# Kernel tuning notes

Hardware: AMD Instinct MI355X
Metric: run time of the kernel (lower is better)

The kernel has to match this reference:

```python
import jax, jax.numpy as jnp
import numpy as np

B, S, H, P = 4, 4096, 1024, 10

def setup_inputs() -> dict:
    key = jax.random.key(0)
    k1, k2, k3, k4, k5 = jax.random.split(key, 5)
    return {
        "query": jax.random.normal(k1, (B, S, H), dtype=jnp.float32),
        "key": jax.random.normal(k2, (B, S, H), dtype=jnp.float32),
        "value": jax.random.normal(k3, (B, S, H), dtype=jnp.float32),
        "prefix_k": jax.random.normal(k4, (P, H), dtype=jnp.float32),
        "prefix_v": jax.random.normal(k5, (P, H), dtype=jnp.float32),
    }

def reference(query, key, value, prefix_k, prefix_v):
    # Broadcast learned prefix over batch and concat ahead of real K/V.
    b = query.shape[0]
    pk = jnp.broadcast_to(prefix_k[None], (b,) + prefix_k.shape)  # [B, P, H]
    pv = jnp.broadcast_to(prefix_v[None], (b,) + prefix_v.shape)
    k_all = jnp.concatenate([pk, key], axis=1)    # [B, P+S, H]
    v_all = jnp.concatenate([pv, value], axis=1)  # [B, P+S, H]
    # Raw (unscaled, unmasked) attention, exactly as the torch module does.
    scores = jnp.einsum("bqh,bkh->bqk", query, k_all)  # [B, S, P+S]
    attn = jax.nn.softmax(scores, axis=-1)
    return jnp.einsum("bqk,bkh->bqh", attn, v_all)     # [B, S, H]
```

## Files before the change

### kernel.cpp

```cpp
#include <hip/hip_runtime.h>
#include <cstdint>
#include <cstddef>

#define BB 4
#define SS 4096
#define HH 1024
#define PP 10
#define LL 4106
#define NTILES 129
#define CHUNKS_PB (NTILES * 4096)
#define TILE_ELEMS (4096 * 8)
#define LOG2E 1.44269504088896f

typedef __attribute__((ext_vector_type(8))) _Float16 half8v;
typedef __attribute__((ext_vector_type(4))) float float4v;

union hu16 { _Float16 h; unsigned short u; };

__device__ __forceinline__ half8v cvt8h(float4v f0, float4v f1) {
  half8v h;
  h[0] = (_Float16)f0[0]; h[1] = (_Float16)f0[1];
  h[2] = (_Float16)f0[2]; h[3] = (_Float16)f0[3];
  h[4] = (_Float16)f1[0]; h[5] = (_Float16)f1[1];
  h[6] = (_Float16)f1[2]; h[7] = (_Float16)f1[3];
  return h;
}
__device__ __forceinline__ unsigned pack2h(float a, float b) {
  hu16 x, y; x.h = (_Float16)a; y.h = (_Float16)b;
  return (unsigned)x.u | ((unsigned)y.u << 16);
}

#define LGKM_BAR() do { \
  asm volatile("s_waitcnt lgkmcnt(0)" ::: "memory"); \
  __builtin_amdgcn_s_barrier(); \
  asm volatile("" ::: "memory"); } while (0)

__global__ __launch_bounds__(256) void conv_k(const float* __restrict__ prefix_k,
                                              const float* __restrict__ key,
                                              _Float16* __restrict__ kp) {
  const int b = blockIdx.y;
  const int id = blockIdx.x * 256 + threadIdx.x;
  const int li = id & 15, g = (id >> 4) & 3, ktp = (id >> 6) & 31,
            nt = (id >> 11) & 1, it = id >> 12;
  const int n = it * 32 + nt * 16 + li;
  const int d = ktp * 32 + g * 8;
  float4v f0 = {0.f, 0.f, 0.f, 0.f}, f1 = {0.f, 0.f, 0.f, 0.f};
  if (n < LL) {
    const float* src = (n < PP) ? prefix_k + (size_t)n * HH + d
                                : key + ((size_t)b * SS + (n - PP)) * HH + d;
    f0 = *(const float4v*)src; f1 = *(const float4v*)(src + 4);
  }
  *(half8v*)(kp + ((size_t)b * CHUNKS_PB + id) * 8) = cvt8h(f0, f1);
}

__global__ __launch_bounds__(256) void conv_v(const float* __restrict__ prefix_v,
                                              const float* __restrict__ value,
                                              _Float16* __restrict__ vp) {
  const int b = blockIdx.y;
  const int id = blockIdx.x * 256 + threadIdx.x;
  const int d = id & 1023, g = (id >> 10) & 3, it = id >> 12;
  const int nb = it * 32 + g * 8;
  half8v h;
  #pragma unroll
  for (int j = 0; j < 8; ++j) {
    int n = nb + j;
    float f = 0.f;
    if (n < LL)
      f = (n < PP) ? prefix_v[(size_t)n * HH + d]
                   : value[((size_t)b * SS + (n - PP)) * HH + d];
    h[j] = (_Float16)f;
  }
  *(half8v*)(vp + ((size_t)b * CHUNKS_PB + id) * 8) = h;
}

template<int PATH>
__global__ __launch_bounds__(512, 2) void attn_fused(
    const float* __restrict__ q,
    const float* __restrict__ key,
    const float* __restrict__ value,
    const float* __restrict__ prefix_k,
    const float* __restrict__ prefix_v,
    const _Float16* __restrict__ kp,
    const _Float16* __restrict__ vp,
    float* __restrict__ out)
{
  __shared__ __align__(16) float sbuf[2][8][32][36];
  __shared__ __align__(16) unsigned short Pl[2][32][40];
  __shared__ float sc_l[2][32];
  __shared__ float l_l[32];

  const int tid = threadIdx.x;
  const int w = tid >> 6, ln = tid & 63, g = ln >> 4, li = ln & 15;
  const int bid = blockIdx.x, xcd = bid & 7, b = xcd >> 1;
  const int qt = ((bid >> 3) << 1) | (xcd & 1);
  const int q0 = qt * 32;
  const int dbase = w * 128;

  half8v qf[2][4];
  #pragma unroll
  for (int mt = 0; mt < 2; ++mt)
    #pragma unroll
    for (int kt = 0; kt < 4; ++kt) {
      const float* p = q + ((size_t)(b * SS + q0 + mt * 16 + li)) * HH + dbase + kt * 32 + g * 8;
      qf[mt][kt] = cvt8h(*(const float4v*)p, *(const float4v*)(p + 4));
    }

  float4v z4 = {0.f, 0.f, 0.f, 0.f};
  float4v o[2][8];
  #pragma unroll
  for (int mt = 0; mt < 2; ++mt)
    #pragma unroll
    for (int dt = 0; dt < 8; ++dt) o[mt][dt] = z4;
  float m_r = -1e30f, l_r = 0.f;

  const _Float16* kbase = kp + ((size_t)b * CHUNKS_PB + (size_t)(w * 4) * 64 + g * 16 + li) * 8;
  const _Float16* vbase = vp + ((size_t)b * CHUNKS_PB + (size_t)g * 1024 + dbase + li) * 8;

  half8v kreg[8];
  half8v vreg[8];
  if constexpr (PATH == 0) {
    #pragma unroll
    for (int kt = 0; kt < 4; ++kt)
      #pragma unroll
      for (int nt = 0; nt < 2; ++nt)
        kreg[kt * 2 + nt] = *(const half8v*)(kbase + (size_t)(nt * 2048 + kt * 64) * 8);
  }

  const int srow = w * 4 + (ln >> 4);
  const int c0 = (ln & 15) * 2;

  for (int i = 0; i < NTILES + 2; ++i) {
    const int sb = i & 1;
    const int ob = sb ^ 1;

    if (i < NTILES) {
      float4v sacc[2][2];
      sacc[0][0] = z4; sacc[0][1] = z4; sacc[1][0] = z4; sacc[1][1] = z4;
      __builtin_amdgcn_s_setprio(1);
      #pragma unroll
      for (int kt = 0; kt < 4; ++kt) {
        half8v kb[2];
        if constexpr (PATH == 0) {
          kb[0] = kreg[kt * 2 + 0]; kb[1] = kreg[kt * 2 + 1];
        } else {
          #pragma unroll
          for (int nt = 0; nt < 2; ++nt) {
            int n = i * 32 + nt * 16 + li;
            int nc = (n < LL) ? n : 0;
            const float* kpp = (nc < PP) ? (prefix_k + (size_t)nc * HH)
                                         : (key + ((size_t)b * SS + (nc - PP)) * HH);
            kpp += dbase + kt * 32 + g * 8;
            kb[nt] = cvt8h(*(const float4v*)kpp, *(const float4v*)(kpp + 4));
          }
        }
        #pragma unroll
        for (int mt = 0; mt < 2; ++mt)
          #pragma unroll
          for (int nt = 0; nt < 2; ++nt)
            sacc[mt][nt] = __builtin_amdgcn_mfma_f32_16x16x32_f16(qf[mt][kt], kb[nt], sacc[mt][nt], 0, 0, 0);
      }
      __builtin_amdgcn_s_setprio(0);
      #pragma unroll
      for (int mt = 0; mt < 2; ++mt)
        #pragma unroll
        for (int nt = 0; nt < 2; ++nt)
          #pragma unroll
          for (int r = 0; r < 4; ++r)
            sbuf[sb][w][mt * 16 + g * 4 + r][nt * 16 + li] = sacc[mt][nt][r];
      if constexpr (PATH == 0) {
        kbase += TILE_ELEMS;
        #pragma unroll
        for (int kt = 0; kt < 4; ++kt)
          #pragma unroll
          for (int nt = 0; nt < 2; ++nt)
            kreg[kt * 2 + nt] = *(const half8v*)(kbase + (size_t)(nt * 2048 + kt * 64) * 8);
      }
    }

    if (i >= 1 && i <= NTILES) {
      const int t = i - 1;
      float s0 = 0.f, s1 = 0.f;
      #pragma unroll
      for (int bw = 0; bw < 8; ++bw) {
        float2 tv = *(const float2*)&sbuf[ob][bw][srow][c0];
        s0 += tv.x; s1 += tv.y;
      }
      if constexpr (PATH == 1) {
        if (t * 32 + c0 >= LL)     s0 = -1e30f;
        if (t * 32 + c0 + 1 >= LL) s1 = -1e30f;
      }
      float mx = fmaxf(s0, s1);
      mx = fmaxf(mx, __shfl_xor(mx, 1));
      mx = fmaxf(mx, __shfl_xor(mx, 2));
      mx = fmaxf(mx, __shfl_xor(mx, 4));
      mx = fmaxf(mx, __shfl_xor(mx, 8));
      const float m_new = fmaxf(m_r, mx);
      const float scp = exp2f((m_r - m_new) * LOG2E);
      const float p0 = exp2f((s0 - m_new) * LOG2E);
      const float p1 = exp2f((s1 - m_new) * LOG2E);
      float ts = p0 + p1;
      ts += __shfl_xor(ts, 1);
      ts += __shfl_xor(ts, 2);
      ts += __shfl_xor(ts, 4);
      ts += __shfl_xor(ts, 8);
      l_r = l_r * scp + ts;
      m_r = m_new;
      *(unsigned*)&Pl[ob][srow][c0] = pack2h(p0, p1);
      if ((ln & 15) == 0) sc_l[ob][srow] = scp;
    }

    if (i >= 2) {
      const int t = i - 2;
      float scc[2][4];
      #pragma unroll
      for (int mt = 0; mt < 2; ++mt)
        #pragma unroll
        for (int r = 0; r < 4; ++r)
          scc[mt][r] = sc_l[sb][mt * 16 + g * 4 + r];
      #pragma unroll
      for (int mt = 0; mt < 2; ++mt)
        #pragma unroll
        for (int dt = 0; dt < 8; ++dt)
          #pragma unroll
          for (int r = 0; r < 4; ++r)
            o[mt][dt][r] *= scc[mt][r];

      half8v pa0 = *(const half8v*)&Pl[sb][li][g * 8];
      half8v pa1 = *(const half8v*)&Pl[sb][16 + li][g * 8];
      __builtin_amdgcn_s_setprio(1);
      #pragma unroll
      for (int dt = 0; dt < 8; ++dt) {
        half8v vb;
        if constexpr (PATH == 0) {
          vb = vreg[dt];
        } else {
          const int d = dbase + dt * 16 + li;
          #pragma unroll
          for (int j = 0; j < 8; ++j) {
            int n = t * 32 + g * 8 + j;
            int nc = (n < LL) ? n : 0;
            float f = (nc < PP) ? prefix_v[(size_t)nc * HH + d]
                                : value[((size_t)b * SS + (nc - PP)) * HH + d];
            vb[j] = (_Float16)f;
          }
        }
        o[0][dt] = __builtin_amdgcn_mfma_f32_16x16x32_f16(pa0, vb, o[0][dt], 0, 0, 0);
        o[1][dt] = __builtin_amdgcn_mfma_f32_16x16x32_f16(pa1, vb, o[1][dt], 0, 0, 0);
      }
      __builtin_amdgcn_s_setprio(0);
    }

    if constexpr (PATH == 0) {
      if (i >= 1 && i <= NTILES) {
        #pragma unroll
        for (int dt = 0; dt < 8; ++dt)
          vreg[dt] = *(const half8v*)(vbase + (size_t)(dt * 16) * 8);
        vbase += TILE_ELEMS;
      }
    }

    LGKM_BAR();
  }

  if ((ln & 15) == 0) l_l[srow] = l_r;
  LGKM_BAR();
  float il[2][4];
  #pragma unroll
  for (int mt = 0; mt < 2; ++mt)
    #pragma unroll
    for (int r = 0; r < 4; ++r)
      il[mt][r] = 1.0f / l_l[mt * 16 + g * 4 + r];
  #pragma unroll
  for (int mt = 0; mt < 2; ++mt)
    #pragma unroll
    for (int dt = 0; dt < 8; ++dt)
      #pragma unroll
      for (int r = 0; r < 4; ++r)
        out[((size_t)(b * SS + q0 + mt * 16 + g * 4 + r)) * HH + dbase + dt * 16 + li]
            = o[mt][dt][r] * il[mt][r];
}

extern "C" void kernel_launch(void* const* d_in, const int* in_sizes, int n_in,
                              void* d_out, int out_size, void* d_ws, size_t ws_size,
                              hipStream_t stream) {
  const float* q        = (const float*)d_in[0];
  const float* key      = (const float*)d_in[1];
  const float* value    = (const float*)d_in[2];
  const float* prefix_k = (const float*)d_in[3];
  const float* prefix_v = (const float*)d_in[4];
  float* out = (float*)d_out;

  const size_t PLANE = (size_t)BB * CHUNKS_PB * 8;
  const size_t NEED  = 2 * PLANE * sizeof(unsigned short);

  if (ws_size >= NEED) {
    _Float16* kp = (_Float16*)d_ws;
    _Float16* vp = kp + PLANE;
    conv_k<<<dim3(CHUNKS_PB / 256, BB), 256, 0, stream>>>(prefix_k, key, kp);
    conv_v<<<dim3(CHUNKS_PB / 256, BB), 256, 0, stream>>>(prefix_v, value, vp);
    attn_fused<0><<<512, 512, 0, stream>>>(q, key, value, prefix_k, prefix_v, kp, vp, out);
  } else {
    attn_fused<1><<<512, 512, 0, stream>>>(q, key, value, prefix_k, prefix_v,
                                           nullptr, nullptr, out);
  }
}
```

Baseline: 472.6 us.

## Defer softmax max rescaling with threshold and peel pipelined attention loop

Adds lazy online-softmax rescaling: when every lane's new tile max stays within a threshold of the running max, the running max is kept and the scale factor is 1, so the exp of the correction and the rescale of the output accumulators can be skipped (the PV step checks the scale factors and only rescales if any differ from 1). The three-stage software pipeline loop is also peeled into prologue, steady-state and epilogue, removing per-iteration stage guards, and the setprio hints are dropped. Deferred rescaling lets probabilities grow to exp(8) before normalization, which risks fp16 overflow or precision loss in the packed P values when scores are large.

```diff
diff --git a/kernel.cpp b/kernel.cpp
--- a/kernel.cpp
+++ b/kernel.cpp
@@ -11,6 +11,7 @@
 #define CHUNKS_PB (NTILES * 4096)
 #define TILE_ELEMS (4096 * 8)
 #define LOG2E 1.44269504088896f
+#define DEFER_THR 8.0f
 
 typedef __attribute__((ext_vector_type(8))) _Float16 half8v;
 typedef __attribute__((ext_vector_type(4))) float float4v;
@@ -129,94 +130,98 @@
   const int srow = w * 4 + (ln >> 4);
   const int c0 = (ln & 15) * 2;
 
-  for (int i = 0; i < NTILES + 2; ++i) {
-    const int sb = i & 1;
-    const int ob = sb ^ 1;
-
-    if (i < NTILES) {
-      float4v sacc[2][2];
-      sacc[0][0] = z4; sacc[0][1] = z4; sacc[1][0] = z4; sacc[1][1] = z4;
-      __builtin_amdgcn_s_setprio(1);
-      #pragma unroll
-      for (int kt = 0; kt < 4; ++kt) {
-        half8v kb[2];
-        if constexpr (PATH == 0) {
-          kb[0] = kreg[kt * 2 + 0]; kb[1] = kreg[kt * 2 + 1];
-        } else {
-          #pragma unroll
-          for (int nt = 0; nt < 2; ++nt) {
-            int n = i * 32 + nt * 16 + li;
-            int nc = (n < LL) ? n : 0;
-            const float* kpp = (nc < PP) ? (prefix_k + (size_t)nc * HH)
-                                         : (key + ((size_t)b * SS + (nc - PP)) * HH);
-            kpp += dbase + kt * 32 + g * 8;
-            kb[nt] = cvt8h(*(const float4v*)kpp, *(const float4v*)(kpp + 4));
-          }
+  auto do_qk = [&](int i) __attribute__((always_inline)) {
+    float4v sacc[2][2];
+    sacc[0][0] = z4; sacc[0][1] = z4; sacc[1][0] = z4; sacc[1][1] = z4;
+    #pragma unroll
+    for (int kt = 0; kt < 4; ++kt) {
+      half8v kb[2];
+      if constexpr (PATH == 0) {
+        kb[0] = kreg[kt * 2 + 0]; kb[1] = kreg[kt * 2 + 1];
+      } else {
+        #pragma unroll
+        for (int nt = 0; nt < 2; ++nt) {
+          int n = i * 32 + nt * 16 + li;
+          int nc = (n < LL) ? n : 0;
+          const float* kpp = (nc < PP) ? (prefix_k + (size_t)nc * HH)
+                                       : (key + ((size_t)b * SS + (nc - PP)) * HH);
+          kpp += dbase + kt * 32 + g * 8;
+          kb[nt] = cvt8h(*(const float4v*)kpp, *(const float4v*)(kpp + 4));
         }
-        #pragma unroll
-        for (int mt = 0; mt < 2; ++mt)
-          #pragma unroll
-          for (int nt = 0; nt < 2; ++nt)
-            sacc[mt][nt] = __builtin_amdgcn_mfma_f32_16x16x32_f16(qf[mt][kt], kb[nt], sacc[mt][nt], 0, 0, 0);
       }
-      __builtin_amdgcn_s_setprio(0);
       #pragma unroll
       for (int mt = 0; mt < 2; ++mt)
         #pragma unroll
         for (int nt = 0; nt < 2; ++nt)
-          #pragma unroll
-          for (int r = 0; r < 4; ++r)
-            sbuf[sb][w][mt * 16 + g * 4 + r][nt * 16 + li] = sacc[mt][nt][r];
-      if constexpr (PATH == 0) {
-        kbase += TILE_ELEMS;
-        #pragma unroll
-        for (int kt = 0; kt < 4; ++kt)
-          #pragma unroll
-          for (int nt = 0; nt < 2; ++nt)
-            kreg[kt * 2 + nt] = *(const half8v*)(kbase + (size_t)(nt * 2048 + kt * 64) * 8);
+          sacc[mt][nt] = __builtin_amdgcn_mfma_f32_16x16x32_f16(qf[mt][kt], kb[nt], sacc[mt][nt], 0, 0, 0);
+    }
+    #pragma unroll
+    for (int mt = 0; mt < 2; ++mt)
+      #pragma unroll
+      for (int nt = 0; nt < 2; ++nt)
+        #pragma unroll
+        for (int r = 0; r < 4; ++r)
+          sbuf[i & 1][w][mt * 16 + g * 4 + r][nt * 16 + li] = sacc[mt][nt][r];
+    if constexpr (PATH == 0) {
+      kbase += TILE_ELEMS;
+      #pragma unroll
+      for (int kt = 0; kt < 4; ++kt)
+        #pragma unroll
+        for (int nt = 0; nt < 2; ++nt)
+          kreg[kt * 2 + nt] = *(const half8v*)(kbase + (size_t)(nt * 2048 + kt * 64) * 8);
+    }
+  };
+
+  auto do_softmax = [&](int t) __attribute__((always_inline)) {
+    const int bk = t & 1;
+    float s0 = 0.f, s1 = 0.f;
+    #pragma unroll
+    for (int bw = 0; bw < 8; ++bw) {
+      float2 tv = *(const float2*)&sbuf[bk][bw][srow][c0];
+      s0 += tv.x; s1 += tv.y;
+    }
+    if constexpr (PATH == 1) {
+      if (t * 32 + c0 >= LL)     s0 = -1e30f;
+      if (t * 32 + c0 + 1 >= LL) s1 = -1e30f;
+    }
+    float mx = fmaxf(s0, s1);
+    mx = fmaxf(mx, __shfl_xor(mx, 1));
+    mx = fmaxf(mx, __shfl_xor(mx, 2));
+    mx = fmaxf(mx, __shfl_xor(mx, 4));
+    mx = fmaxf(mx, __shfl_xor(mx, 8));
+    const bool stable = (mx <= m_r + DEFER_THR);
+    float m_new, scp;
+    if (__ballot(stable) == 0xFFFFFFFFFFFFFFFFull) {
+      m_new = m_r; scp = 1.0f;
+    } else {
+      m_new = fmaxf(m_r, mx);
+      scp = exp2f((m_r - m_new) * LOG2E);
+    }
+    const float p0 = exp2f((s0 - m_new) * LOG2E);
+    const float p1 = exp2f((s1 - m_new) * LOG2E);
+    float ts = p0 + p1;
+    ts += __shfl_xor(ts, 1);
+    ts += __shfl_xor(ts, 2);
+    ts += __shfl_xor(ts, 4);
+    ts += __shfl_xor(ts, 8);
+    l_r = l_r * scp + ts;
+    m_r = m_new;
+    *(unsigned*)&Pl[bk][srow][c0] = pack2h(p0, p1);
+    if ((ln & 15) == 0) sc_l[bk][srow] = scp;
+  };
+
+  auto do_pv = [&](int t) __attribute__((always_inline)) {
+    const int bk = t & 1;
+    float scc[2][4];
+    bool need = false;
+    #pragma unroll
+    for (int mt = 0; mt < 2; ++mt)
+      #pragma unroll
+      for (int r = 0; r < 4; ++r) {
+        scc[mt][r] = sc_l[bk][mt * 16 + g * 4 + r];
+        need = need || (scc[mt][r] != 1.0f);
       }
-    }
-
-    if (i >= 1 && i <= NTILES) {
-      const int t = i - 1;
-      float s0 = 0.f, s1 = 0.f;
-      #pragma unroll
-      for (int bw = 0; bw < 8; ++bw) {
-        float2 tv = *(const float2*)&sbuf[ob][bw][srow][c0];
-        s0 += tv.x; s1 += tv.y;
-      }
-      if constexpr (PATH == 1) {
-        if (t * 32 + c0 >= LL)     s0 = -1e30f;
-        if (t * 32 + c0 + 1 >= LL) s1 = -1e30f;
-      }
-      float mx = fmaxf(s0, s1);
-      mx = fmaxf(mx, __shfl_xor(mx, 1));
-      mx = fmaxf(mx, __shfl_xor(mx, 2));
-      mx = fmaxf(mx, __shfl_xor(mx, 4));
-      mx = fmaxf(mx, __shfl_xor(mx, 8));
-      const float m_new = fmaxf(m_r, mx);
-      const float scp = exp2f((m_r - m_new) * LOG2E);
-      const float p0 = exp2f((s0 - m_new) * LOG2E);
-      const float p1 = exp2f((s1 - m_new) * LOG2E);
-      float ts = p0 + p1;
-      ts += __shfl_xor(ts, 1);
-      ts += __shfl_xor(ts, 2);
-      ts += __shfl_xor(ts, 4);
-      ts += __shfl_xor(ts, 8);
-      l_r = l_r * scp + ts;
-      m_r = m_new;
-      *(unsigned*)&Pl[ob][srow][c0] = pack2h(p0, p1);
-      if ((ln & 15) == 0) sc_l[ob][srow] = scp;
-    }
-
-    if (i >= 2) {
-      const int t = i - 2;
-      float scc[2][4];
-      #pragma unroll
-      for (int mt = 0; mt < 2; ++mt)
-        #pragma unroll
-        for (int r = 0; r < 4; ++r)
-          scc[mt][r] = sc_l[sb][mt * 16 + g * 4 + r];
+    if (__any(need)) {
       #pragma unroll
       for (int mt = 0; mt < 2; ++mt)
         #pragma unroll
@@ -224,43 +229,53 @@
           #pragma unroll
           for (int r = 0; r < 4; ++r)
             o[mt][dt][r] *= scc[mt][r];
-
-      half8v pa0 = *(const half8v*)&Pl[sb][li][g * 8];
-      half8v pa1 = *(const half8v*)&Pl[sb][16 + li][g * 8];
-      __builtin_amdgcn_s_setprio(1);
-      #pragma unroll
-      for (int dt = 0; dt < 8; ++dt) {
-        half8v vb;
-        if constexpr (PATH == 0) {
-          vb = vreg[dt];
-        } else {
-          const int d = dbase + dt * 16 + li;
-          #pragma unroll
-          for (int j = 0; j < 8; ++j) {
-            int n = t * 32 + g * 8 + j;
-            int nc = (n < LL) ? n : 0;
-            float f = (nc < PP) ? prefix_v[(size_t)nc * HH + d]
-                                : value[((size_t)b * SS + (nc - PP)) * HH + d];
-            vb[j] = (_Float16)f;
-          }
+    }
+    half8v pa0 = *(const half8v*)&Pl[bk][li][g * 8];
+    half8v pa1 = *(const half8v*)&Pl[bk][16 + li][g * 8];
+    #pragma unroll
+    for (int dt = 0; dt < 8; ++dt) {
+      half8v vb;
+      if constexpr (PATH == 0) {
+        vb = vreg[dt];
+      } else {
+        const int d = dbase + dt * 16 + li;
+        #pragma unroll
+        for (int j = 0; j < 8; ++j) {
+          int n = t * 32 + g * 8 + j;
+          int nc = (n < LL) ? n : 0;
+          float f = (nc < PP) ? prefix_v[(size_t)nc * HH + d]
+                              : value[((size_t)b * SS + (nc - PP)) * HH + d];
+          vb[j] = (_Float16)f;
         }
-        o[0][dt] = __builtin_amdgcn_mfma_f32_16x16x32_f16(pa0, vb, o[0][dt], 0, 0, 0);
-        o[1][dt] = __builtin_amdgcn_mfma_f32_16x16x32_f16(pa1, vb, o[1][dt], 0, 0, 0);
       }
-      __builtin_amdgcn_s_setprio(0);
-    }
-
+      o[0][dt] = __builtin_amdgcn_mfma_f32_16x16x32_f16(pa0, vb, o[0][dt], 0, 0, 0);
+      o[1][dt] = __builtin_amdgcn_mfma_f32_16x16x32_f16(pa1, vb, o[1][dt], 0, 0, 0);
+    }
+  };
+
+  auto load_v = [&](int) __attribute__((always_inline)) {
     if constexpr (PATH == 0) {
-      if (i >= 1 && i <= NTILES) {
-        #pragma unroll
-        for (int dt = 0; dt < 8; ++dt)
-          vreg[dt] = *(const half8v*)(vbase + (size_t)(dt * 16) * 8);
-        vbase += TILE_ELEMS;
-      }
-    }
-
+      #pragma unroll
+      for (int dt = 0; dt < 8; ++dt)
+        vreg[dt] = *(const half8v*)(vbase + (size_t)(dt * 16) * 8);
+      vbase += TILE_ELEMS;
+    }
+  };
+
+  do_qk(0);
+  LGKM_BAR();
+  do_qk(1); do_softmax(0); load_v(0);
+  LGKM_BAR();
+  for (int i = 2; i < NTILES; ++i) {
+    do_qk(i);
+    do_softmax(i - 1);
+    do_pv(i - 2);
+    load_v(i - 1);
     LGKM_BAR();
   }
+  do_softmax(NTILES - 1); do_pv(NTILES - 2); load_v(NTILES - 1);
+  LGKM_BAR();
+  do_pv(NTILES - 1);
 
   if ((ln & 15) == 0) l_l[srow] = l_r;
   LGKM_BAR();
```

Result: faster. 436.9 us (-7.6%).
